# Optimization experiments

Measured on AMD Instinct MI355X. Metric: run time of the kernel, lower is better.

The kernel has to match this reference:

```python
import jax, jax.numpy as jnp
import numpy as np

EPS = 1e-5

def setup_inputs() -> dict:
    key = jax.random.key(0)
    ks = jax.random.split(key, 6)
    N, E, C, H, L = 50000, 800000, 128, 128, 3
    x = jax.random.normal(ks[0], (N, C), dtype=jnp.float32)
    edge_index = jax.random.randint(ks[1], (2, E), 0, N, dtype=jnp.int64)
    # Xavier-ish scaled weights; layer 0 uses in=C=H so all layers stack uniformly.
    Wl = jax.random.normal(ks[2], (L, C, H), dtype=jnp.float32) / np.sqrt(C)
    Wr = jax.random.normal(ks[3], (L, C, H), dtype=jnp.float32) / np.sqrt(C)
    b = jnp.zeros((L, H), dtype=jnp.float32)
    gamma = jnp.ones((L, H), dtype=jnp.float32)
    beta = jnp.zeros((L, H), dtype=jnp.float32)
    return {"x": x, "edge_index": edge_index, "Wl": Wl, "Wr": Wr, "b": b,
            "gamma": gamma, "beta": beta}

def _sage_bn_relu(x, src, dst, Wl, Wr, b, gamma, beta):
    N = x.shape[0]
    # mean aggregation of source features into target nodes (PyG SAGEConv default)
    agg = jax.ops.segment_sum(x[src], dst, num_segments=N)          # [N, C]
    deg = jax.ops.segment_sum(jnp.ones_like(dst, dtype=x.dtype), dst, num_segments=N)
    mean_nbr = agg / jnp.maximum(deg, 1.0)[:, None]
    h = mean_nbr @ Wl + x @ Wr + b                                   # [N, H]
    # BatchNorm1d (training-mode batch statistics over nodes)
    mu = jnp.mean(h, axis=0)
    var = jnp.var(h, axis=0)
    h = gamma * (h - mu) * jax.lax.rsqrt(var + EPS) + beta
    return jax.nn.relu(h)  # dropout omitted (deterministic reference, p->0)

def reference(x, edge_index, Wl, Wr, b, gamma, beta):
    src, dst = edge_index[0], edge_index[1]
    h = x
    for l in range(Wl.shape[0]):
        h = _sage_bn_relu(h, src, dst, Wl[l], Wr[l], b[l], gamma[l], beta[l])
    return h
```

## Files before the change

### kernel.cpp

```cpp
#include <hip/hip_runtime.h>
#include <hip/hip_bf16.h>

#define BN_EPS 1e-5f
#define BCAP 16384

typedef unsigned short u16;
typedef unsigned int u32;
typedef __attribute__((ext_vector_type(8))) short bf16x8v;
typedef __attribute__((ext_vector_type(4))) float f32x4v;

__device__ __forceinline__ float bf2f(u16 u){
    union { u32 i; float f; } c; c.i = ((u32)u) << 16; return c.f;
}
__device__ __forceinline__ u16 f2bf(float f){
    union { float f; u32 i; } c; c.f = f;
    u32 x = c.i;
    u32 r = x + 0x7FFFu + ((x >> 16) & 1u);
    return (u16)(r >> 16);
}
__device__ __forceinline__ float lo16(u32 u){
    union { u32 i; float f; } c; c.i = u << 16; return c.f;
}
__device__ __forceinline__ float hi16(u32 u){
    union { u32 i; float f; } c; c.i = u & 0xFFFF0000u; return c.f;
}
__device__ __forceinline__ u32 pack2(float f0, float f1){
    return (u32)f2bf(f0) | ((u32)f2bf(f1) << 16);
}

__global__ void detect_k(const int* __restrict__ ei, const u16* __restrict__ xu,
                         int* __restrict__ flags){
    int lane = threadIdx.x;
    unsigned long long bal = __ballot(ei[2 * lane + 1] != 0);
    int cnt = 0;
    #pragma unroll
    for (int k = 0; k < 4; ++k){
        u16 u = xu[2 * (lane + 64 * k)];
        int e = (u >> 7) & 0xFF;
        cnt += (e >= 0x70 && e <= 0x86) ? 1 : 0;
    }
    #pragma unroll
    for (int off = 1; off < 64; off <<= 1) cnt += __shfl_xor(cnt, off);
    if (lane == 0){
        flags[0] = (bal == 0ULL) ? 1 : 0;
        flags[1] = (cnt >= 128) ? 1 : 0;
    }
}

__global__ void prep_k(const void* __restrict__ x, const void* __restrict__ Wl,
                       const void* __restrict__ Wr, const void* __restrict__ b,
                       const void* __restrict__ g, const void* __restrict__ be,
                       u16* __restrict__ xb, u16* __restrict__ wT, float* __restrict__ p,
                       float* __restrict__ ss0, int total4, int wtot, int per,
                       const int* __restrict__ flags){
    int i = blockIdx.x * blockDim.x + threadIdx.x;
    int bf = flags[1];
    if (i < total4){
        if (bf){
            ((uint2*)xb)[i] = ((const uint2*)x)[i];
        } else {
            float4 v = ((const float4*)x)[i];
            ushort4 o; o.x = f2bf(v.x); o.y = f2bf(v.y); o.z = f2bf(v.z); o.w = f2bf(v.w);
            ((ushort4*)xb)[i] = o;
        }
    }
    if (i < wtot){
        u16 vl = bf ? ((const u16*)Wl)[i] : f2bf(((const float*)Wl)[i]);
        u16 vr = bf ? ((const u16*)Wr)[i] : f2bf(((const float*)Wr)[i]);
        int l = i >> 14, r = (i >> 7) & 127, c = i & 127;
        wT[(size_t)(l * 2 + 0) * 16384 + c * 128 + r] = vl;
        wT[(size_t)(l * 2 + 1) * 16384 + c * 128 + r] = vr;
    }
    if (i < per){
        if (i < 128){ ss0[i] = 1.f; ss0[128 + i] = 0.f; }
        if (bf){
            p[i]           = bf2f(((const u16*)b)[i]);
            p[per + i]     = bf2f(((const u16*)g)[i]);
            p[2 * per + i] = bf2f(((const u16*)be)[i]);
        } else {
            p[i]           = ((const float*)b)[i];
            p[per + i]     = ((const float*)g)[i];
            p[2 * per + i] = ((const float*)be)[i];
        }
    }
}


__global__ __launch_bounds__(1024) void phist_k(const void* __restrict__ ei, int E,
                                                int tile, u32* __restrict__ blockHist,
                                                const int* __restrict__ flags){
    __shared__ u32 lh[128];
    int tid = threadIdx.x;
    if (tid < 128) lh[tid] = 0u;
    __syncthreads();
    int start = blockIdx.x * tile;
    int end = min(E, start + tile);
    int i64 = flags[0];
    for (int i = start + tid; i < end; i += 1024){
        int d = i64 ? (int)((const long long*)ei)[E + i] : ((const int*)ei)[E + i];
        atomicAdd(&lh[d >> 9], 1u);
    }
    __syncthreads();
    if (tid < 128) blockHist[blockIdx.x * 128 + tid] = lh[tid];
}

__global__ void bases_k(const u32* __restrict__ blockHist, u32* __restrict__ blockBase,
                        int* __restrict__ rangeBase, int* __restrict__ rowptrN, int nb){
    __shared__ u32 t_s[128];
    int k = threadIdx.x;
    u32 run = 0;
    for (int b = 0; b < nb; ++b){
        blockBase[b * 128 + k] = run;
        run += blockHist[b * 128 + k];
    }
    t_s[k] = min(run, (u32)BCAP);
    __syncthreads();
    if (k == 0){
        u32 r = 0;
        for (int j = 0; j < 128; ++j){ u32 v = t_s[j]; t_s[j] = r; r += v; }
        rangeBase[128] = (int)r;
        *rowptrN = (int)r;
    }
    __syncthreads();
    rangeBase[k] = (int)t_s[k];
}

__global__ __launch_bounds__(1024) void pscat_k(const void* __restrict__ ei, int E,
                                                int tile, const u32* __restrict__ blockBase,
                                                u32* __restrict__ part,
                                                const int* __restrict__ flags){
    __shared__ u32 lcur[128];
    int tid = threadIdx.x;
    if (tid < 128) lcur[tid] = blockBase[blockIdx.x * 128 + tid];
    __syncthreads();
    int start = blockIdx.x * tile;
    int end = min(E, start + tile);
    int i64 = flags[0];
    for (int i = start + tid; i < end; i += 1024){
        int s, d;
        if (i64){
            const long long* p = (const long long*)ei;
            s = (int)p[i]; d = (int)p[E + i];
        } else {
            const int* p = (const int*)ei;
            s = p[i]; d = p[E + i];
        }
        int k = d >> 9;
        u32 pos = atomicAdd(&lcur[k], 1u);
        if (pos < BCAP) part[(size_t)k * BCAP + pos] = (u32)(u16)s | ((u32)(d & 511) << 16);
    }
}

__global__ __launch_bounds__(1024) void build_k(const u32* __restrict__ part,
                                                const int* __restrict__ rangeBase,
                                                int* __restrict__ rowptr,
                                                float* __restrict__ dinv,
                                                u16* __restrict__ col, int N){
    __shared__ u32 bins[512];
    __shared__ u32 wsum[8];
    __shared__ u16 sorted[BCAP];
    int k   = blockIdx.x;
    int tid = threadIdx.x;
    int base = rangeBase[k];
    int cntk = rangeBase[k + 1] - base;
    int d0   = k << 9;
    if (tid < 512) bins[tid] = 0u;
    __syncthreads();
    const u32* pk = part + (size_t)k * BCAP;
    for (int i = tid; i < cntk; i += 1024)
        atomicAdd(&bins[pk[i] >> 16], 1u);
    __syncthreads();
    int lane = tid & 63, w = tid >> 6;
    u32 v = (tid < 512) ? bins[tid] : 0u;
    u32 sc = v;
    #pragma unroll
    for (int off = 1; off < 64; off <<= 1){
        u32 u = __shfl_up(sc, off);
        if (lane >= off) sc += u;
    }
    if (lane == 63 && w < 8) wsum[w] = sc;
    __syncthreads();
    if (tid == 0){
        u32 r = 0;
        #pragma unroll
        for (int j = 0; j < 8; ++j){ u32 t = wsum[j]; wsum[j] = r; r += t; }
    }
    __syncthreads();
    u32 excl = (w < 8 ? wsum[w] : 0u) + sc - v;
    if (tid < 512){
        int d = d0 + tid;
        if (d < N){
            rowptr[d] = base + (int)excl;
            dinv[d] = 1.f / fmaxf((float)v, 1.f);
        }
        bins[tid] = excl;
    }
    __syncthreads();
    for (int i = tid; i < cntk; i += 1024){
        u32 e = pk[i];
        u32 pos = atomicAdd(&bins[e >> 16], 1u);
        sorted[pos] = (u16)e;
    }
    __syncthreads();
    for (int i = tid; i < cntk; i += 1024)
        col[base + i] = sorted[i];
}

__global__ void agg_k(const u16* __restrict__ h, const float* __restrict__ ssT, int relu,
                      const int* __restrict__ rowptr, const u16* __restrict__ col,
                      const float* __restrict__ dinv, u16* __restrict__ meanb, int N){
    int wid  = (blockIdx.x * blockDim.x + threadIdx.x) >> 6;
    int lane = threadIdx.x & 63;
    if (wid >= N) return;
    int q   = lane >> 4;
    int sub = lane & 15;
    float sc[8], sh[8];
    #pragma unroll
    for (int j = 0; j < 8; ++j){
        sc[j] = ssT[sub * 8 + j];
        sh[j] = ssT[128 + sub * 8 + j];
    }
    int s = rowptr[wid], e = rowptr[wid + 1];
    float a[8] = {0.f,0.f,0.f,0.f,0.f,0.f,0.f,0.f};
    int i = s + q;
    for (; i + 4 < e; i += 8){
        int sn0 = col[i], sn1 = col[i + 4];
        uint4 v0 = *(const uint4*)(h + (size_t)sn0 * 128 + sub * 8);
        uint4 v1 = *(const uint4*)(h + (size_t)sn1 * 128 + sub * 8);
        float f0[8], f1[8];
        f0[0]=lo16(v0.x); f0[1]=hi16(v0.x); f0[2]=lo16(v0.y); f0[3]=hi16(v0.y);
        f0[4]=lo16(v0.z); f0[5]=hi16(v0.z); f0[6]=lo16(v0.w); f0[7]=hi16(v0.w);
        f1[0]=lo16(v1.x); f1[1]=hi16(v1.x); f1[2]=lo16(v1.y); f1[3]=hi16(v1.y);
        f1[4]=lo16(v1.z); f1[5]=hi16(v1.z); f1[6]=lo16(v1.w); f1[7]=hi16(v1.w);
        #pragma unroll
        for (int j = 0; j < 8; ++j){
            float t0 = f0[j] * sc[j] + sh[j];
            float t1 = f1[j] * sc[j] + sh[j];
            if (relu){ t0 = fmaxf(t0, 0.f); t1 = fmaxf(t1, 0.f); }
            a[j] += t0 + t1;
        }
    }
    if (i < e){
        int sn = col[i];
        uint4 v = *(const uint4*)(h + (size_t)sn * 128 + sub * 8);
        float f[8];
        f[0]=lo16(v.x); f[1]=hi16(v.x); f[2]=lo16(v.y); f[3]=hi16(v.y);
        f[4]=lo16(v.z); f[5]=hi16(v.z); f[6]=lo16(v.w); f[7]=hi16(v.w);
        #pragma unroll
        for (int j = 0; j < 8; ++j){
            float t = f[j] * sc[j] + sh[j];
            if (relu) t = fmaxf(t, 0.f);
            a[j] += t;
        }
    }
    #pragma unroll
    for (int off = 16; off < 64; off <<= 1){
        #pragma unroll
        for (int j = 0; j < 8; ++j) a[j] += __shfl_xor(a[j], off);
    }
    if (q == 0){
        float di = dinv[wid];
        uint4 o;
        o.x = pack2(a[0] * di, a[1] * di);
        o.y = pack2(a[2] * di, a[3] * di);
        o.z = pack2(a[4] * di, a[5] * di);
        o.w = pack2(a[6] * di, a[7] * di);
        *(uint4*)(meanb + (size_t)wid * 128 + sub * 8) = o;
    }
}

__global__ __launch_bounds__(256) void gemm_k(
        const u16* __restrict__ Aa, const u16* __restrict__ Ab,
        const float* __restrict__ ssT, int relu,
        const u16* __restrict__ wT, const float* __restrict__ bias,
        u16* __restrict__ hp16, float* __restrict__ stats, int N){
    __shared__ float s_stat[256];
    __shared__ float s_ss[256];
    int tid  = threadIdx.x;
    int lane = tid & 63;
    int w    = tid >> 6;
    int wid  = blockIdx.x * 4 + w;
    int hl   = lane & 15;
    int quad = lane >> 4;
    int m0   = wid * 32;
    s_stat[tid] = 0.f;
    s_ss[tid]   = ssT[tid];
    __syncthreads();

    f32x4v acc[2][8];
    #pragma unroll
    for (int r2 = 0; r2 < 2; ++r2)
        #pragma unroll
        for (int t = 0; t < 8; ++t) acc[r2][t] = (f32x4v){0.f, 0.f, 0.f, 0.f};

    if (m0 < N){
        const u16* arow0[2];
        const u16* arow1[2];
        #pragma unroll
        for (int r2 = 0; r2 < 2; ++r2){
            int rb = m0 + r2 * 16;
            if (rb + 16 > N) rb = N - 16;
            arow0[r2] = Aa + (size_t)(rb + hl) * 128 + quad * 8;
            arow1[r2] = Ab + (size_t)(rb + hl) * 128 + quad * 8;
        }
        {
            const u16* Bp = wT + (size_t)hl * 128 + quad * 8;
            #pragma unroll
            for (int kc = 0; kc < 128; kc += 32){
                bf16x8v af0 = *(const bf16x8v*)(arow0[0] + kc);
                bf16x8v af1 = *(const bf16x8v*)(arow0[1] + kc);
                #pragma unroll
                for (int t = 0; t < 8; ++t){
                    bf16x8v bf = *(const bf16x8v*)(Bp + t * 2048 + kc);
                    acc[0][t] = __builtin_amdgcn_mfma_f32_16x16x32_bf16(af0, bf, acc[0][t], 0, 0, 0);
                    acc[1][t] = __builtin_amdgcn_mfma_f32_16x16x32_bf16(af1, bf, acc[1][t], 0, 0, 0);
                }
            }
        }
        {
            const u16* Bp = wT + 16384 + (size_t)hl * 128 + quad * 8;
            #pragma unroll
            for (int kc = 0; kc < 128; kc += 32){
                int kb = quad * 8 + kc;
                float tsc[8], tsh[8];
                #pragma unroll
                for (int j = 0; j < 8; ++j){
                    tsc[j] = s_ss[kb + j];
                    tsh[j] = s_ss[128 + kb + j];
                }
                bf16x8v afr[2];
                #pragma unroll
                for (int r2 = 0; r2 < 2; ++r2){
                    uint4 raw = *(const uint4*)(arow1[r2] + kc);
                    float f[8];
                    f[0]=lo16(raw.x); f[1]=hi16(raw.x); f[2]=lo16(raw.y); f[3]=hi16(raw.y);
                    f[4]=lo16(raw.z); f[5]=hi16(raw.z); f[6]=lo16(raw.w); f[7]=hi16(raw.w);
                    float t8[8];
                    #pragma unroll
                    for (int j = 0; j < 8; ++j){
                        float t = f[j] * tsc[j] + tsh[j];
                        if (relu) t = fmaxf(t, 0.f);
                        t8[j] = t;
                    }
                    union { bf16x8v v; u32 u[4]; } fr;
                    fr.u[0] = pack2(t8[0], t8[1]);
                    fr.u[1] = pack2(t8[2], t8[3]);
                    fr.u[2] = pack2(t8[4], t8[5]);
                    fr.u[3] = pack2(t8[6], t8[7]);
                    afr[r2] = fr.v;
                }
                #pragma unroll
                for (int t = 0; t < 8; ++t){
                    bf16x8v bf = *(const bf16x8v*)(Bp + t * 2048 + kc);
                    acc[0][t] = __builtin_amdgcn_mfma_f32_16x16x32_bf16(afr[0], bf, acc[0][t], 0, 0, 0);
                    acc[1][t] = __builtin_amdgcn_mfma_f32_16x16x32_bf16(afr[1], bf, acc[1][t], 0, 0, 0);
                }
            }
        }
    }

    #pragma unroll
    for (int r2 = 0; r2 < 2; ++r2){
        int mb = m0 + r2 * 16;
        bool valid = (mb < N);
        #pragma unroll
        for (int t = 0; t < 8; ++t){
            int c = t * 16 + hl;
            float bv = bias[c];
            float cs = 0.f, cq = 0.f;
            if (valid){
                #pragma unroll
                for (int r = 0; r < 4; ++r){
                    float v = acc[r2][t][r] + bv;
                    hp16[(size_t)(mb + quad * 4 + r) * 128 + c] = f2bf(v);
                    cs += v; cq += v * v;
                }
            }
            cs += __shfl_xor(cs, 16); cs += __shfl_xor(cs, 32);
            cq += __shfl_xor(cq, 16); cq += __shfl_xor(cq, 32);
            if (quad == 0 && valid){
                atomicAdd(&s_stat[c], cs);
                atomicAdd(&s_stat[128 + c], cq);
            }
        }
    }
    __syncthreads();
    float* st = stats + (size_t)(blockIdx.x & 63) * 256;
    atomicAdd(&st[tid], s_stat[tid]);
}

__global__ void finalize_k(float* __restrict__ stats, const float* __restrict__ g,
                           const float* __restrict__ be, float* __restrict__ ss, float invN){
    int j = threadIdx.x;
    float s = 0.f, sq = 0.f;
    #pragma unroll 8
    for (int bkt = 0; bkt < 64; ++bkt){
        s  += stats[bkt * 256 + j];
        sq += stats[bkt * 256 + 128 + j];
        stats[bkt * 256 + j] = 0.f;
        stats[bkt * 256 + 128 + j] = 0.f;
    }
    float mu  = s * invN;
    float var = sq * invN - mu * mu;
    if (!(mu == mu)) mu = 0.f;
    if (!(var >= 0.f) || !(var == var)) var = 0.f;
    float sc = g[j] * rsqrtf(var + BN_EPS);
    ss[j]       = sc;
    ss[128 + j] = be[j] - mu * sc;
}

__global__ void applyf_k(const u16* __restrict__ in, const float* __restrict__ ss,
                         float* __restrict__ out, int total4){
    int i = blockIdx.x * blockDim.x + threadIdx.x;
    if (i >= total4) return;
    uint2 u = ((const uint2*)in)[i];
    float4 v;
    v.x = lo16(u.x); v.y = hi16(u.x); v.z = lo16(u.y); v.w = hi16(u.y);
    if (!(v.x == v.x)) v.x = 0.f;
    if (!(v.y == v.y)) v.y = 0.f;
    if (!(v.z == v.z)) v.z = 0.f;
    if (!(v.w == v.w)) v.w = 0.f;
    int c = (i & 31) * 4;
    float4 o;
    o.x = fmaxf(v.x * ss[c]     + ss[128 + c], 0.f);
    o.y = fmaxf(v.y * ss[c + 1] + ss[129 + c], 0.f);
    o.z = fmaxf(v.z * ss[c + 2] + ss[130 + c], 0.f);
    o.w = fmaxf(v.w * ss[c + 3] + ss[131 + c], 0.f);
    ((float4*)out)[i] = o;
}

extern "C" void kernel_launch(void* const* d_in, const int* in_sizes, int n_in,
                              void* d_out, int out_size, void* d_ws, size_t ws_size,
                              hipStream_t stream){
    const void* x  = d_in[0];
    const int*  ei = (const int*)d_in[1];
    const void* Wl = d_in[2];
    const void* Wr = d_in[3];
    const void* b  = d_in[4];
    const void* gm = d_in[5];
    const void* bt = d_in[6];
    float* outf = (float*)d_out;

    const int N = in_sizes[0] / 128;
    const int E = in_sizes[1] / 2;
    const int L = in_sizes[2] / 16384;
    const int PB = 128;
    const int TILE = (E + PB - 1) / PB;

    char* wsp = (char*)d_ws;
    size_t off = 0;
    auto alloc = [&](size_t bytes) -> char* {
        char* p = wsp + off;
        off = (off + bytes + 255) & ~(size_t)255;
        return p;
    };
    int*   flags  = (int*)  alloc(16);
    int*   rowptr = (int*)  alloc((size_t)(N + 1) * 4);
    u16*   col    = (u16*)  alloc((size_t)E * 2);
    float* dinv   = (float*)alloc((size_t)N * 4);
    u32*   bHist  = (u32*)  alloc((size_t)PB * 128 * 4);
    u32*   bBase  = (u32*)  alloc((size_t)PB * 128 * 4);
    int*   rangeB = (int*)  alloc((size_t)129 * 4);
    u32*   part   = (u32*)  alloc((size_t)128 * BCAP * 4);
    u16*   wT     = (u16*)  alloc((size_t)L * 2 * 16384 * 2);
    float* pvec   = (float*)alloc((size_t)3 * L * 128 * 4);
    float* ssb    = (float*)alloc((size_t)(L + 1) * 256 * 4);
    u16*   xb     = (u16*)  alloc((size_t)N * 128 * 2);
    u16*   meanb  = (u16*)  alloc((size_t)N * 128 * 2);
    float* stats  = (float*)alloc((size_t)64 * 256 * 4);
    u16*   hpre16 = (u16*)  alloc((size_t)N * 128 * 2);
    u16*   hA     = (u16*)  alloc((size_t)N * 128 * 2);
    u16*   hB     = (u16*)  alloc((size_t)N * 128 * 2);
    (void)ws_size; (void)n_in; (void)out_size;

    detect_k<<<1, 64, 0, stream>>>(ei, (const u16*)x, flags);
    hipMemsetAsync(stats, 0, (size_t)64 * 256 * 4, stream);

    phist_k<<<PB, 1024, 0, stream>>>((const void*)ei, E, TILE, bHist, flags);
    bases_k<<<1, 128, 0, stream>>>(bHist, bBase, rangeB, rowptr + N, PB);
    pscat_k<<<PB, 1024, 0, stream>>>((const void*)ei, E, TILE, bBase, part, flags);
    build_k<<<128, 1024, 0, stream>>>(part, rangeB, rowptr, dinv, col, N);

    prep_k<<<(N * 32 + 255) / 256, 256, 0, stream>>>(x, Wl, Wr, b, gm, bt, xb, wT, pvec,
                                                     ssb, N * 32, L * 16384, L * 128, flags);

    const u16* state = xb;
    int nwaves = (N + 31) / 32;
    int gblocks = (nwaves + 3) / 4;
    for (int l = 0; l < L; ++l){
        int last = (l == L - 1);
        int relu = (l > 0);
        const float* ssT = ssb + (size_t)l * 256;
        u16* nxt = last ? hpre16 : ((l & 1) ? hB : hA);
        agg_k<<<(N + 3) / 4, 256, 0, stream>>>(state, ssT, relu, rowptr, col, dinv,
                                               meanb, N);
        gemm_k<<<gblocks, 256, 0, stream>>>(meanb, state, ssT, relu,
                                            wT + (size_t)l * 2 * 16384, pvec + l * 128,
                                            nxt, stats, N);
        finalize_k<<<1, 128, 0, stream>>>(stats, pvec + (size_t)L * 128 + l * 128,
                                          pvec + (size_t)2 * L * 128 + l * 128,
                                          ssb + (size_t)(l + 1) * 256, 1.f / (float)N);
        state = nxt;
    }
    applyf_k<<<(N * 32 + 255) / 256, 256, 0, stream>>>(hpre16, ssb + (size_t)L * 256,
                                                       outf, N * 32);
}
```

Before: 352.2 us.

## Fuse neighbor aggregation and GEMM into one per-layer kernel via LDS

Merges the gather/mean aggregation kernel and the MFMA GEMM kernel into a single layer kernel. Each 512-thread block aggregates 32 nodes into an LDS tile and then runs the dual GEMM (mean@Wl + x@Wr) over that tile, with 8 waves splitting rows and column quarters. This drops the global meanb round trip and one launch per layer. In exchange, the per-block GEMM tile shrinks and weights are reloaded by every block, and the gather and MFMA phases no longer overlap across kernels.

Result: no change. 355.5 us (+0.9%).

```diff
diff --git a/kernel.cpp b/kernel.cpp
--- a/kernel.cpp
+++ b/kernel.cpp
@@ -85,7 +85,6 @@
     }
 }
 
-
 __global__ __launch_bounds__(1024) void phist_k(const void* __restrict__ ei, int E,
                                                 int tile, u32* __restrict__ blockHist,
                                                 const int* __restrict__ flags){
@@ -206,187 +205,160 @@
         col[base + i] = sorted[i];
 }
 
-__global__ void agg_k(const u16* __restrict__ h, const float* __restrict__ ssT, int relu,
-                      const int* __restrict__ rowptr, const u16* __restrict__ col,
-                      const float* __restrict__ dinv, u16* __restrict__ meanb, int N){
-    int wid  = (blockIdx.x * blockDim.x + threadIdx.x) >> 6;
-    int lane = threadIdx.x & 63;
-    if (wid >= N) return;
-    int q   = lane >> 4;
-    int sub = lane & 15;
-    float sc[8], sh[8];
-    #pragma unroll
-    for (int j = 0; j < 8; ++j){
-        sc[j] = ssT[sub * 8 + j];
-        sh[j] = ssT[128 + sub * 8 + j];
-    }
-    int s = rowptr[wid], e = rowptr[wid + 1];
-    float a[8] = {0.f,0.f,0.f,0.f,0.f,0.f,0.f,0.f};
-    int i = s + q;
-    for (; i + 4 < e; i += 8){
-        int sn0 = col[i], sn1 = col[i + 4];
-        uint4 v0 = *(const uint4*)(h + (size_t)sn0 * 128 + sub * 8);
-        uint4 v1 = *(const uint4*)(h + (size_t)sn1 * 128 + sub * 8);
-        float f0[8], f1[8];
-        f0[0]=lo16(v0.x); f0[1]=hi16(v0.x); f0[2]=lo16(v0.y); f0[3]=hi16(v0.y);
-        f0[4]=lo16(v0.z); f0[5]=hi16(v0.z); f0[6]=lo16(v0.w); f0[7]=hi16(v0.w);
-        f1[0]=lo16(v1.x); f1[1]=hi16(v1.x); f1[2]=lo16(v1.y); f1[3]=hi16(v1.y);
-        f1[4]=lo16(v1.z); f1[5]=hi16(v1.z); f1[6]=lo16(v1.w); f1[7]=hi16(v1.w);
-        #pragma unroll
-        for (int j = 0; j < 8; ++j){
-            float t0 = f0[j] * sc[j] + sh[j];
-            float t1 = f1[j] * sc[j] + sh[j];
-            if (relu){ t0 = fmaxf(t0, 0.f); t1 = fmaxf(t1, 0.f); }
-            a[j] += t0 + t1;
-        }
-    }
-    if (i < e){
-        int sn = col[i];
-        uint4 v = *(const uint4*)(h + (size_t)sn * 128 + sub * 8);
-        float f[8];
-        f[0]=lo16(v.x); f[1]=hi16(v.x); f[2]=lo16(v.y); f[3]=hi16(v.y);
-        f[4]=lo16(v.z); f[5]=hi16(v.z); f[6]=lo16(v.w); f[7]=hi16(v.w);
-        #pragma unroll
-        for (int j = 0; j < 8; ++j){
-            float t = f[j] * sc[j] + sh[j];
-            if (relu) t = fmaxf(t, 0.f);
-            a[j] += t;
-        }
-    }
-    #pragma unroll
-    for (int off = 16; off < 64; off <<= 1){
-        #pragma unroll
-        for (int j = 0; j < 8; ++j) a[j] += __shfl_xor(a[j], off);
-    }
-    if (q == 0){
-        float di = dinv[wid];
-        uint4 o;
-        o.x = pack2(a[0] * di, a[1] * di);
-        o.y = pack2(a[2] * di, a[3] * di);
-        o.z = pack2(a[4] * di, a[5] * di);
-        o.w = pack2(a[6] * di, a[7] * di);
-        *(uint4*)(meanb + (size_t)wid * 128 + sub * 8) = o;
-    }
-}
-
-__global__ __launch_bounds__(256) void gemm_k(
-        const u16* __restrict__ Aa, const u16* __restrict__ Ab,
-        const float* __restrict__ ssT, int relu,
-        const u16* __restrict__ wT, const float* __restrict__ bias,
-        u16* __restrict__ hp16, float* __restrict__ stats, int N){
+__global__ __launch_bounds__(512) void layer_k(
+        const u16* __restrict__ state, const float* __restrict__ ssT, int relu,
+        const int* __restrict__ rowptr, const u16* __restrict__ col,
+        const float* __restrict__ dinv, const u16* __restrict__ wT,
+        const float* __restrict__ bias, u16* __restrict__ hp16,
+        float* __restrict__ stats, int N){
+    __shared__ u16 aT[32][136];
+    __shared__ float s_ss[256];
     __shared__ float s_stat[256];
-    __shared__ float s_ss[256];
     int tid  = threadIdx.x;
     int lane = tid & 63;
     int w    = tid >> 6;
-    int wid  = blockIdx.x * 4 + w;
+    int m0   = blockIdx.x * 32;
+    if (tid < 256){ s_ss[tid] = ssT[tid]; s_stat[tid] = 0.f; }
+    __syncthreads();
+
+    {
+        int q   = lane >> 4;
+        int sub = lane & 15;
+        float sc[8], sh[8];
+        #pragma unroll
+        for (int j = 0; j < 8; ++j){
+            sc[j] = s_ss[sub * 8 + j];
+            sh[j] = s_ss[128 + sub * 8 + j];
+        }
+        #pragma unroll
+        for (int nn = 0; nn < 4; ++nn){
+            int lrow = w * 4 + nn;
+            int node = m0 + lrow;
+            if (node < N){
+                int s = rowptr[node], e = rowptr[node + 1];
+                float a[8] = {0.f,0.f,0.f,0.f,0.f,0.f,0.f,0.f};
+                int i = s + q;
+                for (; i + 4 < e; i += 8){
+                    int sn0 = col[i], sn1 = col[i + 4];
+                    uint4 v0 = *(const uint4*)(state + (size_t)sn0 * 128 + sub * 8);
+                    uint4 v1 = *(const uint4*)(state + (size_t)sn1 * 128 + sub * 8);
+                    float f0[8], f1[8];
+                    f0[0]=lo16(v0.x); f0[1]=hi16(v0.x); f0[2]=lo16(v0.y); f0[3]=hi16(v0.y);
+                    f0[4]=lo16(v0.z); f0[5]=hi16(v0.z); f0[6]=lo16(v0.w); f0[7]=hi16(v0.w);
+                    f1[0]=lo16(v1.x); f1[1]=hi16(v1.x); f1[2]=lo16(v1.y); f1[3]=hi16(v1.y);
+                    f1[4]=lo16(v1.z); f1[5]=hi16(v1.z); f1[6]=lo16(v1.w); f1[7]=hi16(v1.w);
+                    #pragma unroll
+                    for (int j = 0; j < 8; ++j){
+                        float t0 = f0[j] * sc[j] + sh[j];
+                        float t1 = f1[j] * sc[j] + sh[j];
+                        if (relu){ t0 = fmaxf(t0, 0.f); t1 = fmaxf(t1, 0.f); }
+                        a[j] += t0 + t1;
+                    }
+                }
+                if (i < e){
+                    int sn = col[i];
+                    uint4 v = *(const uint4*)(state + (size_t)sn * 128 + sub * 8);
+                    float f[8];
+                    f[0]=lo16(v.x); f[1]=hi16(v.x); f[2]=lo16(v.y); f[3]=hi16(v.y);
+                    f[4]=lo16(v.z); f[5]=hi16(v.z); f[6]=lo16(v.w); f[7]=hi16(v.w);
+                    #pragma unroll
+                    for (int j = 0; j < 8; ++j){
+                        float t = f[j] * sc[j] + sh[j];
+                        if (relu) t = fmaxf(t, 0.f);
+                        a[j] += t;
+                    }
+                }
+                #pragma unroll
+                for (int off = 16; off < 64; off <<= 1){
+                    #pragma unroll
+                    for (int j = 0; j < 8; ++j) a[j] += __shfl_xor(a[j], off);
+                }
+                if (q == 0){
+                    float di = dinv[node];
+                    uint4 o;
+                    o.x = pack2(a[0] * di, a[1] * di);
+                    o.y = pack2(a[2] * di, a[3] * di);
+                    o.z = pack2(a[4] * di, a[5] * di);
+                    o.w = pack2(a[6] * di, a[7] * di);
+                    *(uint4*)(&aT[lrow][sub * 8]) = o;
+                }
+            } else if (q == 0){
+                uint4 z = {0u,0u,0u,0u};
+                *(uint4*)(&aT[lrow][sub * 8]) = z;
+            }
+        }
+    }
+    __syncthreads();
+
     int hl   = lane & 15;
     int quad = lane >> 4;
-    int m0   = wid * 32;
-    s_stat[tid] = 0.f;
-    s_ss[tid]   = ssT[tid];
-    __syncthreads();
-
-    f32x4v acc[2][8];
+    int rh   = w & 1;
+    int cq   = w >> 1;
+    int rowg = m0 + rh * 16 + hl;
+    int ar   = min(rowg, N - 1);
+    const u16* srow = state + (size_t)ar * 128 + quad * 8;
+    const u16* Bp0  = wT + (size_t)(cq * 32 + hl) * 128 + quad * 8;
+
+    f32x4v acc[2];
+    acc[0] = (f32x4v){0.f,0.f,0.f,0.f};
+    acc[1] = (f32x4v){0.f,0.f,0.f,0.f};
+
     #pragma unroll
-    for (int r2 = 0; r2 < 2; ++r2)
+    for (int kc = 0; kc < 128; kc += 32){
+        bf16x8v am = *(const bf16x8v*)(&aT[rh * 16 + hl][quad * 8 + kc]);
+        int kb = quad * 8 + kc;
+        uint4 raw = *(const uint4*)(srow + kc);
+        float f[8];
+        f[0]=lo16(raw.x); f[1]=hi16(raw.x); f[2]=lo16(raw.y); f[3]=hi16(raw.y);
+        f[4]=lo16(raw.z); f[5]=hi16(raw.z); f[6]=lo16(raw.w); f[7]=hi16(raw.w);
+        float t8[8];
         #pragma unroll
-        for (int t = 0; t < 8; ++t) acc[r2][t] = (f32x4v){0.f, 0.f, 0.f, 0.f};
-
-    if (m0 < N){
-        const u16* arow0[2];
-        const u16* arow1[2];
+        for (int j = 0; j < 8; ++j){
+            float t = f[j] * s_ss[kb + j] + s_ss[128 + kb + j];
+            if (relu) t = fmaxf(t, 0.f);
+            t8[j] = t;
+        }
+        union { bf16x8v v; u32 u[4]; } fr;
+        fr.u[0] = pack2(t8[0], t8[1]);
+        fr.u[1] = pack2(t8[2], t8[3]);
+        fr.u[2] = pack2(t8[4], t8[5]);
+        fr.u[3] = pack2(t8[6], t8[7]);
+        bf16x8v as = fr.v;
         #pragma unroll
-        for (int r2 = 0; r2 < 2; ++r2){
-            int rb = m0 + r2 * 16;
-            if (rb + 16 > N) rb = N - 16;
-            arow0[r2] = Aa + (size_t)(rb + hl) * 128 + quad * 8;
-            arow1[r2] = Ab + (size_t)(rb + hl) * 128 + quad * 8;
-        }
-        {
-            const u16* Bp = wT + (size_t)hl * 128 + quad * 8;
+        for (int t = 0; t < 2; ++t){
+            bf16x8v b0 = *(const bf16x8v*)(Bp0 + t * 2048 + kc);
+            bf16x8v b1 = *(const bf16x8v*)(Bp0 + 16384 + t * 2048 + kc);
+            acc[t] = __builtin_amdgcn_mfma_f32_16x16x32_bf16(am, b0, acc[t], 0, 0, 0);
+            acc[t] = __builtin_amdgcn_mfma_f32_16x16x32_bf16(as, b1, acc[t], 0, 0, 0);
+        }
+    }
+
+    bool valid = (m0 + rh * 16 < N);
+    #pragma unroll
+    for (int t = 0; t < 2; ++t){
+        int c = cq * 32 + t * 16 + hl;
+        float bv = bias[c];
+        float cs = 0.f, cqs = 0.f;
+        if (valid){
             #pragma unroll
-            for (int kc = 0; kc < 128; kc += 32){
-                bf16x8v af0 = *(const bf16x8v*)(arow0[0] + kc);
-                bf16x8v af1 = *(const bf16x8v*)(arow0[1] + kc);
-                #pragma unroll
-                for (int t = 0; t < 8; ++t){
-                    bf16x8v bf = *(const bf16x8v*)(Bp + t * 2048 + kc);
-                    acc[0][t] = __builtin_amdgcn_mfma_f32_16x16x32_bf16(af0, bf, acc[0][t], 0, 0, 0);
-                    acc[1][t] = __builtin_amdgcn_mfma_f32_16x16x32_bf16(af1, bf, acc[1][t], 0, 0, 0);
-                }
+            for (int r = 0; r < 4; ++r){
+                float v = acc[t][r] + bv;
+                hp16[(size_t)(m0 + rh * 16 + quad * 4 + r) * 128 + c] = f2bf(v);
+                cs += v; cqs += v * v;
             }
         }
-        {
-            const u16* Bp = wT + 16384 + (size_t)hl * 128 + quad * 8;
-            #pragma unroll
-            for (int kc = 0; kc < 128; kc += 32){
-                int kb = quad * 8 + kc;
-                float tsc[8], tsh[8];
-                #pragma unroll
-                for (int j = 0; j < 8; ++j){
-                    tsc[j] = s_ss[kb + j];
-                    tsh[j] = s_ss[128 + kb + j];
-                }
-                bf16x8v afr[2];
-                #pragma unroll
-                for (int r2 = 0; r2 < 2; ++r2){
-                    uint4 raw = *(const uint4*)(arow1[r2] + kc);
-                    float f[8];
-                    f[0]=lo16(raw.x); f[1]=hi16(raw.x); f[2]=lo16(raw.y); f[3]=hi16(raw.y);
-                    f[4]=lo16(raw.z); f[5]=hi16(raw.z); f[6]=lo16(raw.w); f[7]=hi16(raw.w);
-                    float t8[8];
-                    #pragma unroll
-                    for (int j = 0; j < 8; ++j){
-                        float t = f[j] * tsc[j] + tsh[j];
-                        if (relu) t = fmaxf(t, 0.f);
-                        t8[j] = t;
-                    }
-                    union { bf16x8v v; u32 u[4]; } fr;
-                    fr.u[0] = pack2(t8[0], t8[1]);
-                    fr.u[1] = pack2(t8[2], t8[3]);
-                    fr.u[2] = pack2(t8[4], t8[5]);
-                    fr.u[3] = pack2(t8[6], t8[7]);
-                    afr[r2] = fr.v;
-                }
-                #pragma unroll
-                for (int t = 0; t < 8; ++t){
-                    bf16x8v bf = *(const bf16x8v*)(Bp + t * 2048 + kc);
-                    acc[0][t] = __builtin_amdgcn_mfma_f32_16x16x32_bf16(afr[0], bf, acc[0][t], 0, 0, 0);
-                    acc[1][t] = __builtin_amdgcn_mfma_f32_16x16x32_bf16(afr[1], bf, acc[1][t], 0, 0, 0);
-                }
-            }
-        }
-    }
-
-    #pragma unroll
-    for (int r2 = 0; r2 < 2; ++r2){
-        int mb = m0 + r2 * 16;
-        bool valid = (mb < N);
-        #pragma unroll
-        for (int t = 0; t < 8; ++t){
-            int c = t * 16 + hl;
-            float bv = bias[c];
-            float cs = 0.f, cq = 0.f;
-            if (valid){
-                #pragma unroll
-                for (int r = 0; r < 4; ++r){
-                    float v = acc[r2][t][r] + bv;
-                    hp16[(size_t)(mb + quad * 4 + r) * 128 + c] = f2bf(v);
-                    cs += v; cq += v * v;
-                }
-            }
-            cs += __shfl_xor(cs, 16); cs += __shfl_xor(cs, 32);
-            cq += __shfl_xor(cq, 16); cq += __shfl_xor(cq, 32);
-            if (quad == 0 && valid){
-                atomicAdd(&s_stat[c], cs);
-                atomicAdd(&s_stat[128 + c], cq);
-            }
-        }
-    }
-    __syncthreads();
-    float* st = stats + (size_t)(blockIdx.x & 63) * 256;
-    atomicAdd(&st[tid], s_stat[tid]);
+        cs  += __shfl_xor(cs, 16);  cs  += __shfl_xor(cs, 32);
+        cqs += __shfl_xor(cqs, 16); cqs += __shfl_xor(cqs, 32);
+        if (quad == 0 && valid){
+            atomicAdd(&s_stat[c], cs);
+            atomicAdd(&s_stat[128 + c], cqs);
+        }
+    }
+    __syncthreads();
+    if (tid < 256){
+        float* st = stats + (size_t)(blockIdx.x & 63) * 256;
+        atomicAdd(&st[tid], s_stat[tid]);
+    }
 }
 
 __global__ void finalize_k(float* __restrict__ stats, const float* __restrict__ g,
@@ -466,7 +438,6 @@
     float* pvec   = (float*)alloc((size_t)3 * L * 128 * 4);
     float* ssb    = (float*)alloc((size_t)(L + 1) * 256 * 4);
     u16*   xb     = (u16*)  alloc((size_t)N * 128 * 2);
-    u16*   meanb  = (u16*)  alloc((size_t)N * 128 * 2);
     float* stats  = (float*)alloc((size_t)64 * 256 * 4);
     u16*   hpre16 = (u16*)  alloc((size_t)N * 128 * 2);
     u16*   hA     = (u16*)  alloc((size_t)N * 128 * 2);
@@ -485,18 +456,15 @@
                                                      ssb, N * 32, L * 16384, L * 128, flags);
 
     const u16* state = xb;
-    int nwaves = (N + 31) / 32;
-    int gblocks = (nwaves + 3) / 4;
+    int gblocks = (N + 31) / 32;
     for (int l = 0; l < L; ++l){
         int last = (l == L - 1);
         int relu = (l > 0);
         const float* ssT = ssb + (size_t)l * 256;
         u16* nxt = last ? hpre16 : ((l & 1) ? hB : hA);
-        agg_k<<<(N + 3) / 4, 256, 0, stream>>>(state, ssT, relu, rowptr, col, dinv,
-                                               meanb, N);
-        gemm_k<<<gblocks, 256, 0, stream>>>(meanb, state, ssT, relu,
-                                            wT + (size_t)l * 2 * 16384, pvec + l * 128,
-                                            nxt, stats, N);
+        layer_k<<<gblocks, 512, 0, stream>>>(state, ssT, relu, rowptr, col, dinv,
+                                             wT + (size_t)l * 2 * 16384, pvec + l * 128,
+                                             nxt, stats, N);
         finalize_k<<<1, 128, 0, stream>>>(stats, pvec + (size_t)L * 128 + l * 128,
                                           pvec + (size_t)2 * L * 128 + l * 128,
                                           ssb + (size_t)(l + 1) * 256, 1.f / (float)N);
```

## Materialize BN+ReLU output per layer instead of fusing into agg and gemm

Applied to the files above, without the earlier changes.

The previous BatchNorm scale/shift and ReLU were applied on the fly inside the aggregation gather and the GEMM's right-operand load. They are now applied once per layer by a separate apply kernel, which writes a bf16 activation buffer, or fp32 output on the last layer. The agg and gemm inner loops become pure bf16 sums and MFMA. The cost is an extra full read and write of the N×128 activation per layer plus one more kernel launch.

Result: no change. 350.6 us (-0.5%).

```diff
diff --git a/kernel.cpp b/kernel.cpp
--- a/kernel.cpp
+++ b/kernel.cpp
@@ -51,8 +51,7 @@
                        const void* __restrict__ Wr, const void* __restrict__ b,
                        const void* __restrict__ g, const void* __restrict__ be,
                        u16* __restrict__ xb, u16* __restrict__ wT, float* __restrict__ p,
-                       float* __restrict__ ss0, int total4, int wtot, int per,
-                       const int* __restrict__ flags){
+                       int total4, int wtot, int per, const int* __restrict__ flags){
     int i = blockIdx.x * blockDim.x + threadIdx.x;
     int bf = flags[1];
     if (i < total4){
@@ -72,7 +71,6 @@
         wT[(size_t)(l * 2 + 1) * 16384 + c * 128 + r] = vr;
     }
     if (i < per){
-        if (i < 128){ ss0[i] = 1.f; ss0[128 + i] = 0.f; }
         if (bf){
             p[i]           = bf2f(((const u16*)b)[i]);
             p[per + i]     = bf2f(((const u16*)g)[i]);
@@ -84,7 +82,6 @@
         }
     }
 }
-
 
 __global__ __launch_bounds__(1024) void phist_k(const void* __restrict__ ei, int E,
                                                 int tile, u32* __restrict__ blockHist,
@@ -206,20 +203,14 @@
         col[base + i] = sorted[i];
 }
 
-__global__ void agg_k(const u16* __restrict__ h, const float* __restrict__ ssT, int relu,
-                      const int* __restrict__ rowptr, const u16* __restrict__ col,
-                      const float* __restrict__ dinv, u16* __restrict__ meanb, int N){
+__global__ void agg_k(const u16* __restrict__ h, const int* __restrict__ rowptr,
+                      const u16* __restrict__ col, const float* __restrict__ dinv,
+                      u16* __restrict__ meanb, int N){
     int wid  = (blockIdx.x * blockDim.x + threadIdx.x) >> 6;
     int lane = threadIdx.x & 63;
     if (wid >= N) return;
     int q   = lane >> 4;
     int sub = lane & 15;
-    float sc[8], sh[8];
-    #pragma unroll
-    for (int j = 0; j < 8; ++j){
-        sc[j] = ssT[sub * 8 + j];
-        sh[j] = ssT[128 + sub * 8 + j];
-    }
     int s = rowptr[wid], e = rowptr[wid + 1];
     float a[8] = {0.f,0.f,0.f,0.f,0.f,0.f,0.f,0.f};
     int i = s + q;
@@ -227,31 +218,18 @@
         int sn0 = col[i], sn1 = col[i + 4];
         uint4 v0 = *(const uint4*)(h + (size_t)sn0 * 128 + sub * 8);
         uint4 v1 = *(const uint4*)(h + (size_t)sn1 * 128 + sub * 8);
-        float f0[8], f1[8];
-        f0[0]=lo16(v0.x); f0[1]=hi16(v0.x); f0[2]=lo16(v0.y); f0[3]=hi16(v0.y);
-        f0[4]=lo16(v0.z); f0[5]=hi16(v0.z); f0[6]=lo16(v0.w); f0[7]=hi16(v0.w);
-        f1[0]=lo16(v1.x); f1[1]=hi16(v1.x); f1[2]=lo16(v1.y); f1[3]=hi16(v1.y);
-        f1[4]=lo16(v1.z); f1[5]=hi16(v1.z); f1[6]=lo16(v1.w); f1[7]=hi16(v1.w);
-        #pragma unroll
-        for (int j = 0; j < 8; ++j){
-            float t0 = f0[j] * sc[j] + sh[j];
-            float t1 = f1[j] * sc[j] + sh[j];
-            if (relu){ t0 = fmaxf(t0, 0.f); t1 = fmaxf(t1, 0.f); }
-            a[j] += t0 + t1;
-        }
+        a[0] += lo16(v0.x) + lo16(v1.x); a[1] += hi16(v0.x) + hi16(v1.x);
+        a[2] += lo16(v0.y) + lo16(v1.y); a[3] += hi16(v0.y) + hi16(v1.y);
+        a[4] += lo16(v0.z) + lo16(v1.z); a[5] += hi16(v0.z) + hi16(v1.z);
+        a[6] += lo16(v0.w) + lo16(v1.w); a[7] += hi16(v0.w) + hi16(v1.w);
     }
     if (i < e){
         int sn = col[i];
         uint4 v = *(const uint4*)(h + (size_t)sn * 128 + sub * 8);
-        float f[8];
-        f[0]=lo16(v.x); f[1]=hi16(v.x); f[2]=lo16(v.y); f[3]=hi16(v.y);
-        f[4]=lo16(v.z); f[5]=hi16(v.z); f[6]=lo16(v.w); f[7]=hi16(v.w);
-        #pragma unroll
-        for (int j = 0; j < 8; ++j){
-            float t = f[j] * sc[j] + sh[j];
-            if (relu) t = fmaxf(t, 0.f);
-            a[j] += t;
-        }
+        a[0] += lo16(v.x); a[1] += hi16(v.x);
+        a[2] += lo16(v.y); a[3] += hi16(v.y);
+        a[4] += lo16(v.z); a[5] += hi16(v.z);
+        a[6] += lo16(v.w); a[7] += hi16(v.w);
     }
     #pragma unroll
     for (int off = 16; off < 64; off <<= 1){
@@ -271,11 +249,9 @@
 
 __global__ __launch_bounds__(256) void gemm_k(
         const u16* __restrict__ Aa, const u16* __restrict__ Ab,
-        const float* __restrict__ ssT, int relu,
         const u16* __restrict__ wT, const float* __restrict__ bias,
         u16* __restrict__ hp16, float* __restrict__ stats, int N){
     __shared__ float s_stat[256];
-    __shared__ float s_ss[256];
     int tid  = threadIdx.x;
     int lane = tid & 63;
     int w    = tid >> 6;
@@ -284,7 +260,6 @@
     int quad = lane >> 4;
     int m0   = wid * 32;
     s_stat[tid] = 0.f;
-    s_ss[tid]   = ssT[tid];
     __syncthreads();
 
     f32x4v acc[2][8];
@@ -303,57 +278,20 @@
             arow0[r2] = Aa + (size_t)(rb + hl) * 128 + quad * 8;
             arow1[r2] = Ab + (size_t)(rb + hl) * 128 + quad * 8;
         }
-        {
-            const u16* Bp = wT + (size_t)hl * 128 + quad * 8;
+        #pragma unroll
+        for (int half = 0; half < 2; ++half){
+            const u16* A0 = half ? arow1[0] : arow0[0];
+            const u16* A1 = half ? arow1[1] : arow0[1];
+            const u16* Bp = wT + half * 16384 + (size_t)hl * 128 + quad * 8;
             #pragma unroll
             for (int kc = 0; kc < 128; kc += 32){
-                bf16x8v af0 = *(const bf16x8v*)(arow0[0] + kc);
-                bf16x8v af1 = *(const bf16x8v*)(arow0[1] + kc);
+                bf16x8v af0 = *(const bf16x8v*)(A0 + kc);
+                bf16x8v af1 = *(const bf16x8v*)(A1 + kc);
                 #pragma unroll
                 for (int t = 0; t < 8; ++t){
                     bf16x8v bf = *(const bf16x8v*)(Bp + t * 2048 + kc);
                     acc[0][t] = __builtin_amdgcn_mfma_f32_16x16x32_bf16(af0, bf, acc[0][t], 0, 0, 0);
                     acc[1][t] = __builtin_amdgcn_mfma_f32_16x16x32_bf16(af1, bf, acc[1][t], 0, 0, 0);
-                }
-            }
-        }
-        {
-            const u16* Bp = wT + 16384 + (size_t)hl * 128 + quad * 8;
-            #pragma unroll
-            for (int kc = 0; kc < 128; kc += 32){
-                int kb = quad * 8 + kc;
-                float tsc[8], tsh[8];
-                #pragma unroll
-                for (int j = 0; j < 8; ++j){
-                    tsc[j] = s_ss[kb + j];
-                    tsh[j] = s_ss[128 + kb + j];
-                }
-                bf16x8v afr[2];
-                #pragma unroll
-                for (int r2 = 0; r2 < 2; ++r2){
-                    uint4 raw = *(const uint4*)(arow1[r2] + kc);
-                    float f[8];
-                    f[0]=lo16(raw.x); f[1]=hi16(raw.x); f[2]=lo16(raw.y); f[3]=hi16(raw.y);
-                    f[4]=lo16(raw.z); f[5]=hi16(raw.z); f[6]=lo16(raw.w); f[7]=hi16(raw.w);
-                    float t8[8];
-                    #pragma unroll
-                    for (int j = 0; j < 8; ++j){
-                        float t = f[j] * tsc[j] + tsh[j];
-                        if (relu) t = fmaxf(t, 0.f);
-                        t8[j] = t;
-                    }
-                    union { bf16x8v v; u32 u[4]; } fr;
-                    fr.u[0] = pack2(t8[0], t8[1]);
-                    fr.u[1] = pack2(t8[2], t8[3]);
-                    fr.u[2] = pack2(t8[4], t8[5]);
-                    fr.u[3] = pack2(t8[6], t8[7]);
-                    afr[r2] = fr.v;
-                }
-                #pragma unroll
-                for (int t = 0; t < 8; ++t){
-                    bf16x8v bf = *(const bf16x8v*)(Bp + t * 2048 + kc);
-                    acc[0][t] = __builtin_amdgcn_mfma_f32_16x16x32_bf16(afr[0], bf, acc[0][t], 0, 0, 0);
-                    acc[1][t] = __builtin_amdgcn_mfma_f32_16x16x32_bf16(afr[1], bf, acc[1][t], 0, 0, 0);
                 }
             }
         }
@@ -409,8 +347,9 @@
     ss[128 + j] = be[j] - mu * sc;
 }
 
-__global__ void applyf_k(const u16* __restrict__ in, const float* __restrict__ ss,
-                         float* __restrict__ out, int total4){
+__global__ void apply_k(const u16* __restrict__ in, const float* __restrict__ ss,
+                        u16* __restrict__ outb, float* __restrict__ outf, int use_f32,
+                        int total4){
     int i = blockIdx.x * blockDim.x + threadIdx.x;
     if (i >= total4) return;
     uint2 u = ((const uint2*)in)[i];
@@ -421,12 +360,17 @@
     if (!(v.z == v.z)) v.z = 0.f;
     if (!(v.w == v.w)) v.w = 0.f;
     int c = (i & 31) * 4;
-    float4 o;
-    o.x = fmaxf(v.x * ss[c]     + ss[128 + c], 0.f);
-    o.y = fmaxf(v.y * ss[c + 1] + ss[129 + c], 0.f);
-    o.z = fmaxf(v.z * ss[c + 2] + ss[130 + c], 0.f);
-    o.w = fmaxf(v.w * ss[c + 3] + ss[131 + c], 0.f);
-    ((float4*)out)[i] = o;
+    float r0 = fmaxf(v.x * ss[c]     + ss[128 + c], 0.f);
+    float r1 = fmaxf(v.y * ss[c + 1] + ss[129 + c], 0.f);
+    float r2 = fmaxf(v.z * ss[c + 2] + ss[130 + c], 0.f);
+    float r3 = fmaxf(v.w * ss[c + 3] + ss[131 + c], 0.f);
+    if (use_f32){
+        float4 o; o.x = r0; o.y = r1; o.z = r2; o.w = r3;
+        ((float4*)outf)[i] = o;
+    } else {
+        uint2 o; o.x = pack2(r0, r1); o.y = pack2(r2, r3);
+        ((uint2*)outb)[i] = o;
+    }
 }
 
 extern "C" void kernel_launch(void* const* d_in, const int* in_sizes, int n_in,
@@ -464,7 +408,7 @@
     u32*   part   = (u32*)  alloc((size_t)128 * BCAP * 4);
     u16*   wT     = (u16*)  alloc((size_t)L * 2 * 16384 * 2);
     float* pvec   = (float*)alloc((size_t)3 * L * 128 * 4);
-    float* ssb    = (float*)alloc((size_t)(L + 1) * 256 * 4);
+    float* ss     = (float*)alloc(256 * 4);
     u16*   xb     = (u16*)  alloc((size_t)N * 128 * 2);
     u16*   meanb  = (u16*)  alloc((size_t)N * 128 * 2);
     float* stats  = (float*)alloc((size_t)64 * 256 * 4);
@@ -482,26 +426,22 @@
     build_k<<<128, 1024, 0, stream>>>(part, rangeB, rowptr, dinv, col, N);
 
     prep_k<<<(N * 32 + 255) / 256, 256, 0, stream>>>(x, Wl, Wr, b, gm, bt, xb, wT, pvec,
-                                                     ssb, N * 32, L * 16384, L * 128, flags);
+                                                     N * 32, L * 16384, L * 128, flags);
 
     const u16* state = xb;
     int nwaves = (N + 31) / 32;
     int gblocks = (nwaves + 3) / 4;
     for (int l = 0; l < L; ++l){
         int last = (l == L - 1);
-        int relu = (l > 0);
-        const float* ssT = ssb + (size_t)l * 256;
-        u16* nxt = last ? hpre16 : ((l & 1) ? hB : hA);
-        agg_k<<<(N + 3) / 4, 256, 0, stream>>>(state, ssT, relu, rowptr, col, dinv,
-                                               meanb, N);
-        gemm_k<<<gblocks, 256, 0, stream>>>(meanb, state, ssT, relu,
-                                            wT + (size_t)l * 2 * 16384, pvec + l * 128,
-                                            nxt, stats, N);
+        u16* nxt = (l & 1) ? hB : hA;
+        agg_k<<<(N + 3) / 4, 256, 0, stream>>>(state, rowptr, col, dinv, meanb, N);
+        gemm_k<<<gblocks, 256, 0, stream>>>(meanb, state, wT + (size_t)l * 2 * 16384,
+                                            pvec + l * 128, hpre16, stats, N);
         finalize_k<<<1, 128, 0, stream>>>(stats, pvec + (size_t)L * 128 + l * 128,
                                           pvec + (size_t)2 * L * 128 + l * 128,
-                                          ssb + (size_t)(l + 1) * 256, 1.f / (float)N);
+                                          ss, 1.f / (float)N);
+        apply_k<<<(N * 32 + 255) / 256, 256, 0, stream>>>(hpre16, ss, nxt, outf, last,
+                                                          N * 32);
         state = nxt;
     }
-    applyf_k<<<(N * 32 + 255) / 256, 256, 0, stream>>>(hpre16, ssb + (size_t)L * 256,
-                                                       outf, N * 32);
-}
+}
```
